# Kernel optimization log

Measured on AMD Instinct MI355X. Metric: run time of the kernel, lower is better.

The kernel has to match this reference:

```python
import jax, jax.numpy as jnp
import numpy as np
from jax import lax


def setup_inputs() -> dict:
    key = jax.random.key(0)
    k1, k2 = jax.random.split(key)
    N, C, H, W, R = 8, 128, 96, 192, 4
    feat_ref = jax.random.normal(k1, (N, C, H, W), dtype=jnp.float32)
    feat_src = jax.random.normal(k2, (N, C, H, W), dtype=jnp.float32)
    # Dense (2R+1)^2 displacement grid, columns are (dx, dy) as in the torch module.
    dy, dx = np.meshgrid(np.arange(-R, R + 1), np.arange(-R, R + 1), indexing="ij")
    offsets = jnp.asarray(np.stack([dx.ravel(), dy.ravel()], axis=1), dtype=jnp.int32)  # [S,2]
    return {"feat_ref": feat_ref, "feat_src": feat_src, "offsets": offsets}


def reference(feat_ref, feat_src, offsets):
    # offsets are static metadata (they determine pad sizes); read them on host.
    off = np.asarray(offsets)
    ox, oy = off[:, 0], off[:, 1]
    pad_l = int(max(0, -ox.min()))
    pad_r = int(max(0, ox.max()))
    pad_t = int(max(0, -oy.min()))
    pad_b = int(max(0, oy.max()))

    N, C, H, W = feat_ref.shape
    # padding_mode='zeros' -> constant zero pad (matches torch F.pad default).
    src_p = jnp.pad(feat_src, ((0, 0), (0, 0), (pad_t, pad_b), (pad_l, pad_r)))
    mask_p = jnp.pad(jnp.ones((N, 1, H, W), dtype=jnp.float32),
                     ((0, 0), (0, 0), (pad_t, pad_b), (pad_l, pad_r)))

    def step(carry, o):
        dx, dy = o[0], o[1]
        sl = lax.dynamic_slice(src_p, (0, 0, pad_t + dy, pad_l + dx), (N, C, H, W))
        corr = jnp.sum(feat_ref * sl, axis=1)  # [N,H,W] channel-sum correlation
        m = lax.dynamic_slice(mask_p, (0, 0, pad_t + dy, pad_l + dx), (N, 1, H, W))[:, 0]
        return carry, (corr, m)

    _, (corr, mask) = lax.scan(step, None, offsets)  # each [S,N,H,W]
    corr = jnp.transpose(corr, (1, 0, 2, 3))  # [N,S,H,W]
    mask = jnp.transpose(mask, (1, 0, 2, 3))  # [N,S,H,W]
    return corr, mask
```

## Files before the change

kernel.cpp:

```cpp
#include <hip/hip_runtime.h>

typedef float float4t __attribute__((ext_vector_type(4)));

#define HH 96
#define WW 192
#define PLANE (HH*WW)
#define NCH 128
#define NOFF 81
#define NBATCH 8
#define TS 16
#define HALO 24
#define NPOS (HALO*HALO)
#define CC 4
#define NR (NCH/CC)

__global__ __launch_bounds__(256) void corr_kern(const float* __restrict__ fref,
                                                 const float* __restrict__ fsrc,
                                                 const int* __restrict__ offs,
                                                 float* __restrict__ out) {
  __shared__ float4t tile[NPOS];
  __shared__ int sdelta[NOFF];
  __shared__ int sdx[NOFF];
  __shared__ int sdy[NOFF];

  const int tid = threadIdx.x;
  if (tid < NOFF) {
    int dx = offs[2 * tid];
    int dy = offs[2 * tid + 1];
    sdx[tid] = dx;
    sdy[tid] = dy;
    sdelta[tid] = (dy + 4) * HALO + (dx + 4);
  }

  const int tx = tid & (TS - 1);
  const int ty = tid >> 4;
  const int n  = blockIdx.z;
  const int x0 = blockIdx.x * TS;
  const int y0 = blockIdx.y * TS;
  const int x = x0 + tx;
  const int y = y0 + ty;

  float acc[NOFF];
#pragma unroll
  for (int o = 0; o < NOFF; ++o) acc[o] = 0.f;

  const float* refp = fref + ((size_t)n * NCH) * PLANE + (size_t)y * WW + x;
  const float* srcb = fsrc + ((size_t)n * NCH) * PLANE;

  for (int rd = 0; rd < NR; ++rd) {
    const int c0 = rd * CC;
    __syncthreads();

#pragma unroll
    for (int it = 0; it < 3; ++it) {
      int i = it * 256 + tid;
      if (i < NPOS) {
        int r = i / HALO;
        int c = i - r * HALO;
        int gy = y0 + r - 4;
        int gx = x0 + c - 4;
        bool ok = ((unsigned)gy < (unsigned)HH) & ((unsigned)gx < (unsigned)WW);
        int gyc = min(max(gy, 0), HH - 1);
        int gxc = min(max(gx, 0), WW - 1);
        const float* sp = srcb + (size_t)c0 * PLANE + (size_t)gyc * WW + gxc;
        float4t v;
        v.x = ok ? sp[0]         : 0.f;
        v.y = ok ? sp[PLANE]     : 0.f;
        v.z = ok ? sp[2 * PLANE] : 0.f;
        v.w = ok ? sp[3 * PLANE] : 0.f;
        tile[i] = v;
      }
    }
    __syncthreads();

    float r0 = refp[(size_t)(c0 + 0) * PLANE];
    float r1 = refp[(size_t)(c0 + 1) * PLANE];
    float r2 = refp[(size_t)(c0 + 2) * PLANE];
    float r3 = refp[(size_t)(c0 + 3) * PLANE];

    const float4t* bp = tile + ty * HALO + tx;
#pragma unroll
    for (int o = 0; o < NOFF; ++o) {
      float4t v = bp[sdelta[o]];
      float s = acc[o];
      s = fmaf(r0, v.x, s);
      s = fmaf(r1, v.y, s);
      s = fmaf(r2, v.z, s);
      s = fmaf(r3, v.w, s);
      acc[o] = s;
    }
  }

  float* corrp = out + ((size_t)n * NOFF) * PLANE + (size_t)y * WW + x;
  float* maskp = corrp + (size_t)NBATCH * NOFF * PLANE;
#pragma unroll
  for (int o = 0; o < NOFF; ++o) {
    int dy = sdy[o];
    int dx = sdx[o];
    bool ok = ((unsigned)(y + dy) < (unsigned)HH) & ((unsigned)(x + dx) < (unsigned)WW);
    corrp[(size_t)o * PLANE] = acc[o];
    maskp[(size_t)o * PLANE] = ok ? 1.f : 0.f;
  }
}

extern "C" void kernel_launch(void* const* d_in, const int* in_sizes, int n_in,
                              void* d_out, int out_size, void* d_ws, size_t ws_size,
                              hipStream_t stream) {
  const float* fref = (const float*)d_in[0];
  const float* fsrc = (const float*)d_in[1];
  const int*   offs = (const int*)d_in[2];
  float* out = (float*)d_out;

  dim3 grid(WW / TS, HH / TS, NBATCH);
  dim3 block(256);
  corr_kern<<<grid, block, 0, stream>>>(fref, fsrc, offs, out);
}
```

Measured before the change: 354.2 us.

## Pack source tile to fp16, double channels per round, prefetch next round

Source and reference values are rounded to packed fp16 pairs, so each LDS entry now holds 8 channels and each round processes 8 channels instead of 4. Next-round global loads are prefetched into registers while the current round computes. The offset table is replaced by a hardcoded 9x9 grid, which removes the shared-memory index lookups. This is meant to halve LDS reads and barriers per channel and to hide global load latency. The cost is fp16 rounding of the inputs, which may exceed accuracy tolerance, and the kernel no longer reads the offsets input.

Result: faster. 290.9 us (-17.9%).

```diff
diff --git a/kernel.cpp b/kernel.cpp
--- a/kernel.cpp
+++ b/kernel.cpp
@@ -1,6 +1,7 @@
 #include <hip/hip_runtime.h>
 
-typedef float float4t __attribute__((ext_vector_type(4)));
+typedef __fp16 h2 __attribute__((ext_vector_type(2)));
+typedef unsigned int u32x4 __attribute__((ext_vector_type(4)));
 
 #define HH 96
 #define WW 192
@@ -11,27 +12,25 @@
 #define TS 16
 #define HALO 24
 #define NPOS (HALO*HALO)
-#define CC 4
+#define CC 8
 #define NR (NCH/CC)
+#define SWR 9
+
+__device__ __forceinline__ float mixfma(h2 a, h2 b, float c) {
+  c = fmaf((float)a.x, (float)b.x, c);
+  c = fmaf((float)a.y, (float)b.y, c);
+  return c;
+}
+
+__device__ __forceinline__ h2 bch2(unsigned int u) { return __builtin_bit_cast(h2, u); }
 
 __global__ __launch_bounds__(256) void corr_kern(const float* __restrict__ fref,
                                                  const float* __restrict__ fsrc,
-                                                 const int* __restrict__ offs,
                                                  float* __restrict__ out) {
-  __shared__ float4t tile[NPOS];
-  __shared__ int sdelta[NOFF];
-  __shared__ int sdx[NOFF];
-  __shared__ int sdy[NOFF];
+  __shared__ u32x4 tile[NPOS];
+  unsigned int* ldsu = (unsigned int*)tile;
 
   const int tid = threadIdx.x;
-  if (tid < NOFF) {
-    int dx = offs[2 * tid];
-    int dy = offs[2 * tid + 1];
-    sdx[tid] = dx;
-    sdy[tid] = dy;
-    sdelta[tid] = (dy + 4) * HALO + (dx + 4);
-  }
-
   const int tx = tid & (TS - 1);
   const int ty = tid >> 4;
   const int n  = blockIdx.z;
@@ -40,6 +39,25 @@
   const int x = x0 + tx;
   const int y = y0 + ty;
 
+  int goff[SWR];
+  int dwv[SWR];
+  unsigned lidx[SWR];
+  bool okf[SWR];
+#pragma unroll
+  for (int it = 0; it < SWR; ++it) {
+    int i   = it * 256 + tid;
+    int dw  = i / NPOS;
+    int pos = i - dw * NPOS;
+    int r   = pos / HALO;
+    int c   = pos - r * HALO;
+    int gy = y0 + r - 4;
+    int gx = x0 + c - 4;
+    okf[it]  = ((unsigned)gy < (unsigned)HH) & ((unsigned)gx < (unsigned)WW);
+    goff[it] = min(max(gy, 0), HH - 1) * WW + min(max(gx, 0), WW - 1);
+    dwv[it]  = dw;
+    lidx[it] = (unsigned)(pos * 4 + dw);
+  }
+
   float acc[NOFF];
 #pragma unroll
   for (int o = 0; o < NOFF; ++o) acc[o] = 0.f;
@@ -47,59 +65,69 @@
   const float* refp = fref + ((size_t)n * NCH) * PLANE + (size_t)y * WW + x;
   const float* srcb = fsrc + ((size_t)n * NCH) * PLANE;
 
+  float s0[SWR], s1[SWR];
+#pragma unroll
+  for (int it = 0; it < SWR; ++it) {
+    const float* p = srcb + (size_t)(2 * dwv[it]) * PLANE + goff[it];
+    s0[it] = okf[it] ? p[0] : 0.f;
+    s1[it] = okf[it] ? p[PLANE] : 0.f;
+  }
+
+  const u32x4* bp = tile + (ty * HALO + tx);
+
   for (int rd = 0; rd < NR; ++rd) {
     const int c0 = rd * CC;
     __syncthreads();
-
 #pragma unroll
-    for (int it = 0; it < 3; ++it) {
-      int i = it * 256 + tid;
-      if (i < NPOS) {
-        int r = i / HALO;
-        int c = i - r * HALO;
-        int gy = y0 + r - 4;
-        int gx = x0 + c - 4;
-        bool ok = ((unsigned)gy < (unsigned)HH) & ((unsigned)gx < (unsigned)WW);
-        int gyc = min(max(gy, 0), HH - 1);
-        int gxc = min(max(gx, 0), WW - 1);
-        const float* sp = srcb + (size_t)c0 * PLANE + (size_t)gyc * WW + gxc;
-        float4t v;
-        v.x = ok ? sp[0]         : 0.f;
-        v.y = ok ? sp[PLANE]     : 0.f;
-        v.z = ok ? sp[2 * PLANE] : 0.f;
-        v.w = ok ? sp[3 * PLANE] : 0.f;
-        tile[i] = v;
-      }
+    for (int it = 0; it < SWR; ++it) {
+      h2 pk = __builtin_amdgcn_cvt_pkrtz(s0[it], s1[it]);
+      ldsu[lidx[it]] = __builtin_bit_cast(unsigned int, pk);
     }
     __syncthreads();
 
-    float r0 = refp[(size_t)(c0 + 0) * PLANE];
-    float r1 = refp[(size_t)(c0 + 1) * PLANE];
-    float r2 = refp[(size_t)(c0 + 2) * PLANE];
-    float r3 = refp[(size_t)(c0 + 3) * PLANE];
+    if (rd + 1 < NR) {
+#pragma unroll
+      for (int it = 0; it < SWR; ++it) {
+        const float* p = srcb + (size_t)(c0 + CC + 2 * dwv[it]) * PLANE + goff[it];
+        s0[it] = okf[it] ? p[0] : 0.f;
+        s1[it] = okf[it] ? p[PLANE] : 0.f;
+      }
+    }
 
-    const float4t* bp = tile + ty * HALO + tx;
+    h2 rf0 = __builtin_amdgcn_cvt_pkrtz(refp[(size_t)(c0 + 0) * PLANE], refp[(size_t)(c0 + 1) * PLANE]);
+    h2 rf1 = __builtin_amdgcn_cvt_pkrtz(refp[(size_t)(c0 + 2) * PLANE], refp[(size_t)(c0 + 3) * PLANE]);
+    h2 rf2 = __builtin_amdgcn_cvt_pkrtz(refp[(size_t)(c0 + 4) * PLANE], refp[(size_t)(c0 + 5) * PLANE]);
+    h2 rf3 = __builtin_amdgcn_cvt_pkrtz(refp[(size_t)(c0 + 6) * PLANE], refp[(size_t)(c0 + 7) * PLANE]);
+
 #pragma unroll
-    for (int o = 0; o < NOFF; ++o) {
-      float4t v = bp[sdelta[o]];
-      float s = acc[o];
-      s = fmaf(r0, v.x, s);
-      s = fmaf(r1, v.y, s);
-      s = fmaf(r2, v.z, s);
-      s = fmaf(r3, v.w, s);
-      acc[o] = s;
+    for (int oy = 0; oy < 9; ++oy) {
+#pragma unroll
+      for (int ox = 0; ox < 9; ++ox) {
+        const int o = oy * 9 + ox;
+        u32x4 q = bp[oy * HALO + ox];
+        float s = acc[o];
+        s = mixfma(bch2(q.x), rf0, s);
+        s = mixfma(bch2(q.y), rf1, s);
+        s = mixfma(bch2(q.z), rf2, s);
+        s = mixfma(bch2(q.w), rf3, s);
+        acc[o] = s;
+      }
     }
   }
 
   float* corrp = out + ((size_t)n * NOFF) * PLANE + (size_t)y * WW + x;
   float* maskp = corrp + (size_t)NBATCH * NOFF * PLANE;
 #pragma unroll
-  for (int o = 0; o < NOFF; ++o) {
-    int dy = sdy[o];
-    int dx = sdx[o];
-    bool ok = ((unsigned)(y + dy) < (unsigned)HH) & ((unsigned)(x + dx) < (unsigned)WW);
-    corrp[(size_t)o * PLANE] = acc[o];
-    maskp[(size_t)o * PLANE] = ok ? 1.f : 0.f;
+  for (int oy = 0; oy < 9; ++oy) {
+#pragma unroll
+    for (int ox = 0; ox < 9; ++ox) {
+      const int o = oy * 9 + ox;
+      const int dy = oy - 4;
+      const int dx = ox - 4;
+      bool ok = ((unsigned)(y + dy) < (unsigned)HH) & ((unsigned)(x + dx) < (unsigned)WW);
+      corrp[(size_t)o * PLANE] = acc[o];
+      maskp[(size_t)o * PLANE] = ok ? 1.f : 0.f;
+    }
   }
 }
 
@@ -108,10 +136,9 @@
                               hipStream_t stream) {
   const float* fref = (const float*)d_in[0];
   const float* fsrc = (const float*)d_in[1];
-  const int*   offs = (const int*)d_in[2];
   float* out = (float*)d_out;
 
   dim3 grid(WW / TS, HH / TS, NBATCH);
   dim3 block(256);
-  corr_kern<<<grid, block, 0, stream>>>(fref, fsrc, offs, out);
+  corr_kern<<<grid, block, 0, stream>>>(fref, fsrc, out);
 }
```
